# Kernel optimization log

Measured on AMD Instinct MI355X. Metric: run time of the kernel, lower is better.

Reference implementation:

```python
import jax, jax.numpy as jnp
import numpy as np

N, B, LMAX, M, D, KV, H = 12288, 4, 4096, 1024, 256, 512, 8
EPS = 1e-5


def layernorm(x, g, b):
    mu = jnp.mean(x, axis=-1, keepdims=True)
    var = jnp.mean(jnp.square(x - mu), axis=-1, keepdims=True)
    return (x - mu) * jax.lax.rsqrt(var + EPS) * g + b


def setup_inputs() -> dict:
    key = jax.random.key(0)
    ks = jax.random.split(key, 8)
    s = 0.02
    F = jax.random.normal(ks[0], (N, D), jnp.float32)
    batch_idx = jnp.sort(jax.random.randint(ks[1], (N,), 0, B, dtype=jnp.int32))
    y = jax.random.normal(ks[2], (B, M, KV), jnp.float32)
    Wq = jax.random.normal(ks[3], (D, D), jnp.float32) * s
    Wk = jax.random.normal(ks[4], (D, KV), jnp.float32) * s
    Wv = jax.random.normal(ks[5], (D, KV), jnp.float32) * s
    Wo = jax.random.normal(ks[6], (D, D), jnp.float32) * s
    zb = jnp.zeros((D,), jnp.float32)
    return dict(F=F, batch_idx=batch_idx, y=y,
                Wq=Wq, bq=zb, Wk=Wk, bk=zb, Wv=Wv, bv=zb, Wo=Wo, bo=zb,
                ln_g=jnp.ones((D,), jnp.float32), ln_b=zb, Lmax=LMAX)


def reference(F, batch_idx, y, Wq, bq, Wk, bk, Wv, bv, Wo, bo, ln_g, ln_b, Lmax):
    Bn, Mn, _ = y.shape
    n, d = F.shape
    # sparse_to_dense: scatter points into [B, Lmax, D] by (batch, position-in-batch)
    counts = jax.ops.segment_sum(jnp.ones((n,), jnp.int32), batch_idx, num_segments=Bn)
    starts = jnp.cumsum(counts) - counts                      # first row of each batch
    pos = jnp.arange(n, dtype=jnp.int32) - starts[batch_idx]  # intra-batch position
    xd = jnp.zeros((Bn, Lmax, d), F.dtype).at[batch_idx, pos].set(F)
    # pre-norm (shared LayerNorm params, reused again post-residual)
    q_in = layernorm(xd, ln_g, ln_b)
    # multi-head cross-attention (no key padding mask: mask arg is None here)
    dh = d // H
    q = (q_in @ Wq.T + bq).reshape(Bn, Lmax, H, dh)
    k = (y @ Wk.T + bk).reshape(Bn, Mn, H, dh)
    v = (y @ Wv.T + bv).reshape(Bn, Mn, H, dh)
    scores = jnp.einsum('blhd,bmhd->bhlm', q, k) / jnp.sqrt(jnp.float32(dh))
    p = jax.nn.softmax(scores, axis=-1)
    o = jnp.einsum('bhlm,bmhd->blhd', p, v).reshape(Bn, Lmax, d)
    attn = o @ Wo.T + bo
    # residual on the (normed) query, then the SAME LayerNorm again
    res = layernorm(q_in + attn, ln_g, ln_b)
    # dense_to_sparse: gather valid rows back (row-major order == input order)
    return res[batch_idx, pos]
```

## Files before the change

### kernel.cpp

```cpp
#include <hip/hip_runtime.h>

constexpr int NP = 12288;
constexpr int NB = 4;
constexpr int MC = 1024;
constexpr int DM = 256;
constexpr int KVD = 512;
constexpr int NH = 8;
constexpr int DH = 32;

typedef __bf16 bf16x8 __attribute__((ext_vector_type(8)));
typedef __bf16 bf16x4 __attribute__((ext_vector_type(4)));
typedef float f32x4v __attribute__((ext_vector_type(4)));

__device__ inline bf16x8 pack8(float4 a, float4 b) {
    bf16x8 r;
    r[0] = (__bf16)a.x; r[1] = (__bf16)a.y; r[2] = (__bf16)a.z; r[3] = (__bf16)a.w;
    r[4] = (__bf16)b.x; r[5] = (__bf16)b.y; r[6] = (__bf16)b.z; r[7] = (__bf16)b.w;
    return r;
}

__global__ __launch_bounds__(256) void k_prep(const float* __restrict__ F,
        const int* __restrict__ bidx,
        const float* __restrict__ wq, const float* __restrict__ wk,
        const float* __restrict__ wv, const float* __restrict__ wo,
        const float* __restrict__ g, const float* __restrict__ bb,
        int* __restrict__ starts,
        __bf16* wqb, __bf16* wkb, __bf16* wvb, __bf16* wob,
        __bf16* __restrict__ q_in_b) {
    const int bid = blockIdx.x, t = threadIdx.x;
    if (bid == 0) {
        if (t > NB) return;
        int lo = 0, hi = NP;
        while (lo < hi) { int mid = (lo + hi) >> 1; if (bidx[mid] < t) lo = mid + 1; else hi = mid; }
        starts[t] = lo;
        return;
    }
    if (bid <= 384) {
        size_t i = ((size_t)(bid - 1) * 256 + t) * 4;
        const float* s; __bf16* d; size_t off;
        if      (i < 65536)  { s = wq; d = wqb; off = 0; }
        else if (i < 196608) { s = wk; d = wkb; off = 65536; }
        else if (i < 327680) { s = wv; d = wvb; off = 196608; }
        else                 { s = wo; d = wob; off = 327680; }
        size_t j = i - off;
        float4 v = *(const float4*)&s[j];
        bf16x4 o; o[0] = (__bf16)v.x; o[1] = (__bf16)v.y; o[2] = (__bf16)v.z; o[3] = (__bf16)v.w;
        *(bf16x4*)&d[j] = o;
        return;
    }
    const int w = t >> 6, l = t & 63;
    size_t row = (size_t)(bid - 385) * 4 + w;
    float4 v = *(const float4*)&F[row * DM + l * 4];
    float s = v.x + v.y + v.z + v.w;
#pragma unroll
    for (int o2 = 1; o2 < 64; o2 <<= 1) s += __shfl_xor(s, o2);
    float mu = s * (1.f / DM);
    float4 d = {v.x - mu, v.y - mu, v.z - mu, v.w - mu};
    float ss = d.x * d.x + d.y * d.y + d.z * d.z + d.w * d.w;
#pragma unroll
    for (int o2 = 1; o2 < 64; o2 <<= 1) ss += __shfl_xor(ss, o2);
    float rr = rsqrtf(ss * (1.f / DM) + 1e-5f);
    float4 gg = *(const float4*)&g[l * 4];
    float4 bv = *(const float4*)&bb[l * 4];
    bf16x4 ob4;
    ob4[0] = (__bf16)(d.x * rr * gg.x + bv.x);
    ob4[1] = (__bf16)(d.y * rr * gg.y + bv.y);
    ob4[2] = (__bf16)(d.z * rr * gg.z + bv.z);
    ob4[3] = (__bf16)(d.w * rr * gg.w + bv.w);
    *(bf16x4*)&q_in_b[row * DM + l * 4] = ob4;
}

__global__ __launch_bounds__(256) void k_qkv(const __bf16* __restrict__ Aq,
        const __bf16* __restrict__ Wq, const float* __restrict__ bq,
        const float* __restrict__ Yf,
        const __bf16* __restrict__ Wk, const float* __restrict__ bk,
        const __bf16* __restrict__ Wv, const float* __restrict__ bv,
        __bf16* __restrict__ Qo, __bf16* __restrict__ Kf,
        __bf16* __restrict__ Vf, float qscale) {
    __shared__ __bf16 As[128][68];
    __shared__ __bf16 Bs[64][68];
    const int t = threadIdx.x;
    const int w = t >> 6, l = t & 63, lg = l >> 4, ln = l & 15;
    const int wr = w >> 1, wc = w & 1;
    const int ar = t >> 3, ac8 = (t & 7) * 8;
    if ((int)blockIdx.x < 384) {
        f32x4v acc[4][2] = {};
        const int K = DM;
        const int col0 = (blockIdx.x & 3) * 64, row0 = (blockIdx.x >> 2) * 128;
        bf16x8 ra0, ra1, ra2, ra3, rb0, rb1;
#define LOADGQ(K0) \
        ra0 = *(const bf16x8*)&Aq[(size_t)(row0 + ar) * K + (K0) + ac8];        \
        ra1 = *(const bf16x8*)&Aq[(size_t)(row0 + ar + 32) * K + (K0) + ac8];   \
        ra2 = *(const bf16x8*)&Aq[(size_t)(row0 + ar + 64) * K + (K0) + ac8];   \
        ra3 = *(const bf16x8*)&Aq[(size_t)(row0 + ar + 96) * K + (K0) + ac8];   \
        rb0 = *(const bf16x8*)&Wq[(size_t)(col0 + ar) * K + (K0) + ac8];        \
        rb1 = *(const bf16x8*)&Wq[(size_t)(col0 + ar + 32) * K + (K0) + ac8];
        LOADGQ(0)
        for (int k0 = 0; k0 < K; k0 += 64) {
            __syncthreads();
            *(bf16x8*)&As[ar][ac8] = ra0;
            *(bf16x8*)&As[ar + 32][ac8] = ra1;
            *(bf16x8*)&As[ar + 64][ac8] = ra2;
            *(bf16x8*)&As[ar + 96][ac8] = ra3;
            *(bf16x8*)&Bs[ar][ac8] = rb0;
            *(bf16x8*)&Bs[ar + 32][ac8] = rb1;
            __syncthreads();
            if (k0 + 64 < K) { LOADGQ(k0 + 64) }
#pragma unroll
            for (int kk = 0; kk < 2; ++kk) {
                bf16x8 bfr[2];
#pragma unroll
                for (int ni = 0; ni < 2; ++ni) {
                    bf16x4 lo = *(const bf16x4*)&Bs[wc * 32 + ni * 16 + ln][kk * 32 + lg * 4];
                    bf16x4 hi = *(const bf16x4*)&Bs[wc * 32 + ni * 16 + ln][kk * 32 + 16 + lg * 4];
                    bfr[ni] = __builtin_shufflevector(lo, hi, 0, 1, 2, 3, 4, 5, 6, 7);
                }
#pragma unroll
                for (int mi = 0; mi < 4; ++mi) {
                    bf16x4 lo = *(const bf16x4*)&As[wr * 64 + mi * 16 + ln][kk * 32 + lg * 4];
                    bf16x4 hi = *(const bf16x4*)&As[wr * 64 + mi * 16 + ln][kk * 32 + 16 + lg * 4];
                    bf16x8 af = __builtin_shufflevector(lo, hi, 0, 1, 2, 3, 4, 5, 6, 7);
#pragma unroll
                    for (int ni = 0; ni < 2; ++ni)
                        acc[mi][ni] = __builtin_amdgcn_mfma_f32_16x16x32_bf16(bfr[ni], af, acc[mi][ni], 0, 0, 0);
                }
            }
        }
#undef LOADGQ
#pragma unroll
        for (int mi = 0; mi < 4; ++mi)
#pragma unroll
            for (int ni = 0; ni < 2; ++ni) {
                int cb = col0 + wc * 32 + ni * 16 + 4 * lg;
                float4 b4 = *(const float4*)&bq[cb];
                size_t row = row0 + wr * 64 + mi * 16 + ln;
                bf16x4 pk;
                pk[0] = (__bf16)((acc[mi][ni][0] + b4.x) * qscale);
                pk[1] = (__bf16)((acc[mi][ni][1] + b4.y) * qscale);
                pk[2] = (__bf16)((acc[mi][ni][2] + b4.z) * qscale);
                pk[3] = (__bf16)((acc[mi][ni][3] + b4.w) * qscale);
                *(bf16x4*)&Qo[row * DM + cb] = pk;
            }
    } else {
        f32x4v acc[2][2] = {};
        const int K = KVD;
        const int idx = blockIdx.x - 384;
        const int bx = idx & 7, row0 = (idx >> 3) * 64;
        const bool vpath = bx >= 4;
        const int col0 = (bx & 3) * 64;
        const __bf16* Wm = vpath ? Wv : Wk;
        const float* bi = vpath ? bv : bk;
        float4 a0, a1, a2, a3;
        bf16x8 rb0, rb1;
#define LOADGK(K0) \
        a0 = *(const float4*)&Yf[(size_t)(row0 + ar) * K + (K0) + ac8];            \
        a1 = *(const float4*)&Yf[(size_t)(row0 + ar) * K + (K0) + ac8 + 4];        \
        a2 = *(const float4*)&Yf[(size_t)(row0 + ar + 32) * K + (K0) + ac8];       \
        a3 = *(const float4*)&Yf[(size_t)(row0 + ar + 32) * K + (K0) + ac8 + 4];   \
        rb0 = *(const bf16x8*)&Wm[(size_t)(col0 + ar) * K + (K0) + ac8];           \
        rb1 = *(const bf16x8*)&Wm[(size_t)(col0 + ar + 32) * K + (K0) + ac8];
        LOADGK(0)
        for (int k0 = 0; k0 < K; k0 += 64) {
            __syncthreads();
            *(bf16x8*)&As[ar][ac8] = pack8(a0, a1);
            *(bf16x8*)&As[ar + 32][ac8] = pack8(a2, a3);
            *(bf16x8*)&Bs[ar][ac8] = rb0;
            *(bf16x8*)&Bs[ar + 32][ac8] = rb1;
            __syncthreads();
            if (k0 + 64 < K) { LOADGK(k0 + 64) }
#pragma unroll
            for (int kk = 0; kk < 2; ++kk) {
                bf16x8 bfr[2];
#pragma unroll
                for (int ni = 0; ni < 2; ++ni) {
                    bf16x4 lo = *(const bf16x4*)&Bs[wc * 32 + ni * 16 + ln][kk * 32 + lg * 4];
                    bf16x4 hi = *(const bf16x4*)&Bs[wc * 32 + ni * 16 + ln][kk * 32 + 16 + lg * 4];
                    bfr[ni] = __builtin_shufflevector(lo, hi, 0, 1, 2, 3, 4, 5, 6, 7);
                }
#pragma unroll
                for (int mi = 0; mi < 2; ++mi) {
                    bf16x4 lo = *(const bf16x4*)&As[wr * 32 + mi * 16 + ln][kk * 32 + lg * 4];
                    bf16x4 hi = *(const bf16x4*)&As[wr * 32 + mi * 16 + ln][kk * 32 + 16 + lg * 4];
                    bf16x8 af = __builtin_shufflevector(lo, hi, 0, 1, 2, 3, 4, 5, 6, 7);
#pragma unroll
                    for (int ni = 0; ni < 2; ++ni) {
                        if (vpath)
                            acc[mi][ni] = __builtin_amdgcn_mfma_f32_16x16x32_bf16(af, bfr[ni], acc[mi][ni], 0, 0, 0);
                        else
                            acc[mi][ni] = __builtin_amdgcn_mfma_f32_16x16x32_bf16(bfr[ni], af, acc[mi][ni], 0, 0, 0);
                    }
                }
            }
        }
#undef LOADGK
        if (vpath) {
            const int h = (col0 + wc * 32) >> 5;
#pragma unroll
            for (int mi = 0; mi < 2; ++mi)
#pragma unroll
                for (int ni = 0; ni < 2; ++ni) {
                    int C = col0 + wc * 32 + ni * 16 + ln;
                    int nt = (C >> 4) & 1;
                    float bvv = bi[C];
                    int m = row0 + wr * 32 + mi * 16 + 4 * lg;
                    int b = m >> 10, mlocal = m & 1023;
                    int mhg = mlocal >> 5;
                    bf16x4 pk;
#pragma unroll
                    for (int r = 0; r < 4; ++r) pk[r] = (__bf16)(acc[mi][ni][r] + bvv);
                    *(bf16x4*)&Vf[(size_t)(((b * NH + h) * 32 + mhg) * 2 + nt) * 512 + l * 8 + mi * 4] = pk;
                }
        } else {
            const int h = (col0 + wc * 32) >> 5;
#pragma unroll
            for (int mi = 0; mi < 2; ++mi) {
                int m = row0 + wr * 32 + mi * 16 + ln;
                int b = m >> 10, mlocal = m & 1023;
                int msg = mlocal >> 4;
#pragma unroll
                for (int ni = 0; ni < 2; ++ni) {
                    int cb = col0 + wc * 32 + ni * 16 + 4 * lg;
                    float4 b4 = *(const float4*)&bi[cb];
                    bf16x4 pk;
                    pk[0] = (__bf16)(acc[mi][ni][0] + b4.x);
                    pk[1] = (__bf16)(acc[mi][ni][1] + b4.y);
                    pk[2] = (__bf16)(acc[mi][ni][2] + b4.z);
                    pk[3] = (__bf16)(acc[mi][ni][3] + b4.w);
                    *(bf16x4*)&Kf[(size_t)((b * NH + h) * 64 + msg) * 512 + l * 8 + ni * 4] = pk;
                }
            }
        }
    }
}

__global__ __launch_bounds__(256) void k_attn_mfma(const __bf16* __restrict__ q,
        const __bf16* __restrict__ Kf, const __bf16* __restrict__ Vf,
        const int* __restrict__ starts, __bf16* __restrict__ o) {
    const int b = blockIdx.z, h = blockIdx.y;
    const int r0 = starts[b] + blockIdx.x * 128;
    const int rend = starts[b + 1];
    if (r0 >= rend) return;
    const int nr = min(128, rend - r0);

    const int t = threadIdx.x;
    const int w = t >> 6, l = t & 63, lg = l >> 4, ln = l & 15;

    const __bf16* kfb = Kf + (size_t)(b * NH + h) * 32768;
    const __bf16* vfb = Vf + (size_t)(b * NH + h) * 32768;

    const int qr0 = min(r0 + w * 32 + ln, NP - 1);
    const int qr1 = min(r0 + w * 32 + 16 + ln, NP - 1);
    const __bf16* qp0 = q + (size_t)qr0 * DM + h * DH;
    const __bf16* qp1 = q + (size_t)qr1 * DM + h * DH;
    bf16x8 qf0 = __builtin_shufflevector(*(const bf16x4*)(qp0 + lg * 4),
                                         *(const bf16x4*)(qp0 + 16 + lg * 4),
                                         0, 1, 2, 3, 4, 5, 6, 7);
    bf16x8 qf1 = __builtin_shufflevector(*(const bf16x4*)(qp1 + lg * 4),
                                         *(const bf16x4*)(qp1 + 16 + lg * 4),
                                         0, 1, 2, 3, 4, 5, 6, 7);

    f32x4v OaccA[2] = {{0.f, 0.f, 0.f, 0.f}, {0.f, 0.f, 0.f, 0.f}};
    f32x4v OaccB[2] = {{0.f, 0.f, 0.f, 0.f}, {0.f, 0.f, 0.f, 0.f}};
    float lsA4[4] = {0.f, 0.f, 0.f, 0.f};
    float lsB4[4] = {0.f, 0.f, 0.f, 0.f};

    for (int mt = 0; mt < 8; ++mt) {
        bf16x8 kfr[8];
#pragma unroll
        for (int ms = 0; ms < 8; ++ms)
            kfr[ms] = *(const bf16x8*)&kfb[(size_t)((mt * 8 + ms) * 64 + l) * 8];
        f32x4v S0[8], S1[8];
        __builtin_amdgcn_s_setprio(1);
#pragma unroll
        for (int ms = 0; ms < 8; ++ms) {
            S0[ms] = __builtin_amdgcn_mfma_f32_16x16x32_bf16(
                kfr[ms], qf0, (f32x4v){0.f, 0.f, 0.f, 0.f}, 0, 0, 0);
            S1[ms] = __builtin_amdgcn_mfma_f32_16x16x32_bf16(
                kfr[ms], qf1, (f32x4v){0.f, 0.f, 0.f, 0.f}, 0, 0, 0);
        }
        __builtin_amdgcn_s_setprio(0);
        bf16x8 vfr[8];
#pragma unroll
        for (int i = 0; i < 8; ++i)
            vfr[i] = *(const bf16x8*)&vfb[(size_t)((mt * 8 + i) * 64 + l) * 8];
        bf16x8 pa0[4], pa1[4];
#pragma unroll
        for (int ms = 0; ms < 8; ++ms) {
            const int mh = ms >> 1, j0 = (ms & 1) * 4;
#pragma unroll
            for (int r = 0; r < 4; ++r) {
                float e = __builtin_amdgcn_exp2f(S0[ms][r]);
                lsA4[r] += e;
                pa0[mh][j0 + r] = (__bf16)e;
            }
#pragma unroll
            for (int r = 0; r < 4; ++r) {
                float e = __builtin_amdgcn_exp2f(S1[ms][r]);
                lsB4[r] += e;
                pa1[mh][j0 + r] = (__bf16)e;
            }
        }
        __builtin_amdgcn_s_setprio(1);
#pragma unroll
        for (int mh = 0; mh < 4; ++mh)
#pragma unroll
            for (int nt = 0; nt < 2; ++nt) {
                OaccA[nt] = __builtin_amdgcn_mfma_f32_16x16x32_bf16(pa0[mh], vfr[mh * 2 + nt], OaccA[nt], 0, 0, 0);
                OaccB[nt] = __builtin_amdgcn_mfma_f32_16x16x32_bf16(pa1[mh], vfr[mh * 2 + nt], OaccB[nt], 0, 0, 0);
            }
        __builtin_amdgcn_s_setprio(0);
    }
    float lsA = (lsA4[0] + lsA4[1]) + (lsA4[2] + lsA4[3]);
    float lsB = (lsB4[0] + lsB4[1]) + (lsB4[2] + lsB4[3]);
    lsA += __shfl_xor(lsA, 16); lsA += __shfl_xor(lsA, 32);
    lsB += __shfl_xor(lsB, 16); lsB += __shfl_xor(lsB, 32);
    float invA = 1.0f / lsA, invB = 1.0f / lsB;
    float ivA[4], ivB[4];
#pragma unroll
    for (int r = 0; r < 4; ++r) {
        ivA[r] = __shfl(invA, 4 * lg + r);
        ivB[r] = __shfl(invB, 4 * lg + r);
    }
#pragma unroll
    for (int r = 0; r < 4; ++r) {
        int rlocA = w * 32 + 4 * lg + r;
        if (rlocA < nr) {
            size_t base = (size_t)(r0 + rlocA) * DM + h * DH + ln;
            o[base] = (__bf16)(OaccA[0][r] * ivA[r]);
            o[base + 16] = (__bf16)(OaccA[1][r] * ivA[r]);
        }
        int rlocB = w * 32 + 16 + 4 * lg + r;
        if (rlocB < nr) {
            size_t base = (size_t)(r0 + rlocB) * DM + h * DH + ln;
            o[base] = (__bf16)(OaccB[0][r] * ivB[r]);
            o[base + 16] = (__bf16)(OaccB[1][r] * ivB[r]);
        }
    }
}

__global__ __launch_bounds__(256) void k_gemmo_ln(const __bf16* __restrict__ A,
        const __bf16* __restrict__ W, const float* __restrict__ bias,
        const __bf16* __restrict__ resid, const float* __restrict__ g,
        const float* __restrict__ bb, float* __restrict__ out) {
    __shared__ __bf16 As[32][68];
    __shared__ __bf16 Bs[256][68];
    __shared__ float red[32][4][2];
    const int t = threadIdx.x;
    const int w = t >> 6, l = t & 63, lg = l >> 4, ln = l & 15;
    const int row0 = blockIdx.x * 32;
    const int ar = t >> 3, ac8 = (t & 7) * 8;
    f32x4v acc[2][4] = {};
    for (int k0 = 0; k0 < DM; k0 += 64) {
        __syncthreads();
        *(bf16x8*)&As[ar][ac8] = *(const bf16x8*)&A[(size_t)(row0 + ar) * DM + k0 + ac8];
#pragma unroll
        for (int j = 0; j < 8; ++j)
            *(bf16x8*)&Bs[ar + 32 * j][ac8] = *(const bf16x8*)&W[(size_t)(ar + 32 * j) * DM + k0 + ac8];
        __syncthreads();
#pragma unroll
        for (int kk = 0; kk < 2; ++kk) {
            bf16x8 bfr[4];
#pragma unroll
            for (int ni = 0; ni < 4; ++ni) {
                bf16x4 lo = *(const bf16x4*)&Bs[w * 64 + ni * 16 + ln][kk * 32 + lg * 4];
                bf16x4 hi = *(const bf16x4*)&Bs[w * 64 + ni * 16 + ln][kk * 32 + 16 + lg * 4];
                bfr[ni] = __builtin_shufflevector(lo, hi, 0, 1, 2, 3, 4, 5, 6, 7);
            }
#pragma unroll
            for (int mi = 0; mi < 2; ++mi) {
                bf16x4 lo = *(const bf16x4*)&As[mi * 16 + ln][kk * 32 + lg * 4];
                bf16x4 hi = *(const bf16x4*)&As[mi * 16 + ln][kk * 32 + 16 + lg * 4];
                bf16x8 af = __builtin_shufflevector(lo, hi, 0, 1, 2, 3, 4, 5, 6, 7);
#pragma unroll
                for (int ni = 0; ni < 4; ++ni)
                    acc[mi][ni] = __builtin_amdgcn_mfma_f32_16x16x32_bf16(bfr[ni], af, acc[mi][ni], 0, 0, 0);
            }
        }
    }
    float s[2] = {0.f, 0.f}, ss[2] = {0.f, 0.f};
#pragma unroll
    for (int mi = 0; mi < 2; ++mi) {
        int row = row0 + mi * 16 + ln;
#pragma unroll
        for (int ni = 0; ni < 4; ++ni) {
            int cb = w * 64 + ni * 16 + lg * 4;
            float4 b4 = *(const float4*)&bias[cb];
            bf16x4 rv = *(const bf16x4*)&resid[(size_t)row * DM + cb];
            float z0 = acc[mi][ni][0] + b4.x + (float)rv[0];
            float z1 = acc[mi][ni][1] + b4.y + (float)rv[1];
            float z2 = acc[mi][ni][2] + b4.z + (float)rv[2];
            float z3 = acc[mi][ni][3] + b4.w + (float)rv[3];
            acc[mi][ni][0] = z0; acc[mi][ni][1] = z1;
            acc[mi][ni][2] = z2; acc[mi][ni][3] = z3;
            s[mi] += (z0 + z1) + (z2 + z3);
            ss[mi] += (z0 * z0 + z1 * z1) + (z2 * z2 + z3 * z3);
        }
    }
#pragma unroll
    for (int mi = 0; mi < 2; ++mi) {
        s[mi] += __shfl_xor(s[mi], 16);  s[mi] += __shfl_xor(s[mi], 32);
        ss[mi] += __shfl_xor(ss[mi], 16); ss[mi] += __shfl_xor(ss[mi], 32);
    }
    if (l < 16) {
#pragma unroll
        for (int mi = 0; mi < 2; ++mi) {
            red[mi * 16 + ln][w][0] = s[mi];
            red[mi * 16 + ln][w][1] = ss[mi];
        }
    }
    __syncthreads();
#pragma unroll
    for (int mi = 0; mi < 2; ++mi) {
        int rloc = mi * 16 + ln;
        float su = (red[rloc][0][0] + red[rloc][1][0]) + (red[rloc][2][0] + red[rloc][3][0]);
        float sq = (red[rloc][0][1] + red[rloc][1][1]) + (red[rloc][2][1] + red[rloc][3][1]);
        float mu = su * (1.f / DM);
        float var = sq * (1.f / DM) - mu * mu;
        float rs = rsqrtf(var + 1e-5f);
        size_t row = row0 + rloc;
#pragma unroll
        for (int ni = 0; ni < 4; ++ni) {
            int cb = w * 64 + ni * 16 + lg * 4;
            float4 g4 = *(const float4*)&g[cb];
            float4 bb4 = *(const float4*)&bb[cb];
            float4 o4;
            o4.x = (acc[mi][ni][0] - mu) * rs * g4.x + bb4.x;
            o4.y = (acc[mi][ni][1] - mu) * rs * g4.y + bb4.y;
            o4.z = (acc[mi][ni][2] - mu) * rs * g4.z + bb4.z;
            o4.w = (acc[mi][ni][3] - mu) * rs * g4.w + bb4.w;
            *(float4*)&out[row * DM + cb] = o4;
        }
    }
}

extern "C" void kernel_launch(void* const* d_in, const int* in_sizes, int n_in,
                              void* d_out, int out_size, void* d_ws, size_t ws_size,
                              hipStream_t stream) {
    const float* F  = (const float*)d_in[0];
    const int* bidx = (const int*)d_in[1];
    const float* y  = (const float*)d_in[2];
    const float* Wq = (const float*)d_in[3];
    const float* bq = (const float*)d_in[4];
    const float* Wk = (const float*)d_in[5];
    const float* bk = (const float*)d_in[6];
    const float* Wv = (const float*)d_in[7];
    const float* bv = (const float*)d_in[8];
    const float* Wo = (const float*)d_in[9];
    const float* bo = (const float*)d_in[10];
    const float* lg = (const float*)d_in[11];
    const float* lb = (const float*)d_in[12];
    float* out = (float*)d_out;

    char* ws = (char*)d_ws;
    __bf16* q_in_b = (__bf16*)ws;   ws += (size_t)NP * DM * 2;
    __bf16* qb     = (__bf16*)ws;   ws += (size_t)NP * DM * 2;
    __bf16* ob     = (__bf16*)ws;   ws += (size_t)NP * DM * 2;
    __bf16* Kf     = (__bf16*)ws;   ws += (size_t)NB * MC * DM * 2;
    __bf16* Vf     = (__bf16*)ws;   ws += (size_t)NB * DM * MC * 2;
    __bf16* Wq_b   = (__bf16*)ws;   ws += (size_t)DM * DM * 2;
    __bf16* Wk_b   = (__bf16*)ws;   ws += (size_t)DM * KVD * 2;
    __bf16* Wv_b   = (__bf16*)ws;   ws += (size_t)DM * KVD * 2;
    __bf16* Wo_b   = (__bf16*)ws;   ws += (size_t)DM * DM * 2;
    int* starts    = (int*)ws;

    const float qscale = 0.17677669529663687f * 1.4426950408889634f;

    k_prep<<<1 + 384 + NP / 4, 256, 0, stream>>>(F, bidx, Wq, Wk, Wv, Wo, lg, lb,
            starts, Wq_b, Wk_b, Wv_b, Wo_b, q_in_b);
    k_qkv<<<384 + 512, 256, 0, stream>>>(q_in_b, Wq_b, bq, y, Wk_b, bk, Wv_b, bv,
            qb, Kf, Vf, qscale);
    k_attn_mfma<<<dim3(NP / 128, NH, NB), 256, 0, stream>>>(qb, Kf, Vf, starts, ob);
    k_gemmo_ln<<<NP / 32, 256, 0, stream>>>(ob, Wo_b, bo, q_in_b, lg, lb, out);
}
```

Baseline: 70.70 us.

## Split attention over two key halves and merge partials in output GEMM

The attention grid gains a factor-two split along the key dimension. Each block processes half of the 1024 keys and writes an unnormalised partial output and its per-row exp-sum. The output-projection GEMM loads both partials, adds them, divides by the summed normaliser and then runs its MFMA. This doubles the number of active attention blocks and halves each block's serial loop, at the cost of writing and reading an extra partial output buffer and keeping unnormalised values in bf16.

```diff
diff --git a/kernel.cpp b/kernel.cpp
--- a/kernel.cpp
+++ b/kernel.cpp
@@ -235,8 +235,9 @@
 
 __global__ __launch_bounds__(256) void k_attn_mfma(const __bf16* __restrict__ q,
         const __bf16* __restrict__ Kf, const __bf16* __restrict__ Vf,
-        const int* __restrict__ starts, __bf16* __restrict__ o) {
-    const int b = blockIdx.z, h = blockIdx.y;
+        const int* __restrict__ starts, __bf16* __restrict__ op,
+        float* __restrict__ lsums) {
+    const int z = blockIdx.z, b = z >> 1, half = z & 1, h = blockIdx.y;
     const int r0 = starts[b] + blockIdx.x * 128;
     const int rend = starts[b + 1];
     if (r0 >= rend) return;
@@ -245,8 +246,8 @@
     const int t = threadIdx.x;
     const int w = t >> 6, l = t & 63, lg = l >> 4, ln = l & 15;
 
-    const __bf16* kfb = Kf + (size_t)(b * NH + h) * 32768;
-    const __bf16* vfb = Vf + (size_t)(b * NH + h) * 32768;
+    const __bf16* kfb = Kf + (size_t)(b * NH + h) * 32768 + half * 16384;
+    const __bf16* vfb = Vf + (size_t)(b * NH + h) * 32768 + half * 16384;
 
     const int qr0 = min(r0 + w * 32 + ln, NP - 1);
     const int qr1 = min(r0 + w * 32 + 16 + ln, NP - 1);
@@ -264,7 +265,7 @@
     float lsA4[4] = {0.f, 0.f, 0.f, 0.f};
     float lsB4[4] = {0.f, 0.f, 0.f, 0.f};
 
-    for (int mt = 0; mt < 8; ++mt) {
+    for (int mt = 0; mt < 4; ++mt) {
         bf16x8 kfr[8];
 #pragma unroll
         for (int ms = 0; ms < 8; ++ms)
@@ -314,31 +315,31 @@
     float lsB = (lsB4[0] + lsB4[1]) + (lsB4[2] + lsB4[3]);
     lsA += __shfl_xor(lsA, 16); lsA += __shfl_xor(lsA, 32);
     lsB += __shfl_xor(lsB, 16); lsB += __shfl_xor(lsB, 32);
-    float invA = 1.0f / lsA, invB = 1.0f / lsB;
-    float ivA[4], ivB[4];
-#pragma unroll
-    for (int r = 0; r < 4; ++r) {
-        ivA[r] = __shfl(invA, 4 * lg + r);
-        ivB[r] = __shfl(invB, 4 * lg + r);
+    __bf16* oh = op + (size_t)half * NP * DM;
+    if (l < 16) {
+        int rA = w * 32 + ln, rB = rA + 16;
+        if (rA < nr) lsums[((size_t)half * NP + r0 + rA) * NH + h] = lsA;
+        if (rB < nr) lsums[((size_t)half * NP + r0 + rB) * NH + h] = lsB;
     }
 #pragma unroll
     for (int r = 0; r < 4; ++r) {
         int rlocA = w * 32 + 4 * lg + r;
         if (rlocA < nr) {
             size_t base = (size_t)(r0 + rlocA) * DM + h * DH + ln;
-            o[base] = (__bf16)(OaccA[0][r] * ivA[r]);
-            o[base + 16] = (__bf16)(OaccA[1][r] * ivA[r]);
+            oh[base] = (__bf16)OaccA[0][r];
+            oh[base + 16] = (__bf16)OaccA[1][r];
         }
         int rlocB = w * 32 + 16 + 4 * lg + r;
         if (rlocB < nr) {
             size_t base = (size_t)(r0 + rlocB) * DM + h * DH + ln;
-            o[base] = (__bf16)(OaccB[0][r] * ivB[r]);
-            o[base + 16] = (__bf16)(OaccB[1][r] * ivB[r]);
-        }
-    }
-}
-
-__global__ __launch_bounds__(256) void k_gemmo_ln(const __bf16* __restrict__ A,
+            oh[base] = (__bf16)OaccB[0][r];
+            oh[base + 16] = (__bf16)OaccB[1][r];
+        }
+    }
+}
+
+__global__ __launch_bounds__(256) void k_gemmo_ln(const __bf16* __restrict__ O1,
+        const __bf16* __restrict__ O2, const float* __restrict__ L,
         const __bf16* __restrict__ W, const float* __restrict__ bias,
         const __bf16* __restrict__ resid, const float* __restrict__ g,
         const float* __restrict__ bb, float* __restrict__ out) {
@@ -352,7 +353,18 @@
     f32x4v acc[2][4] = {};
     for (int k0 = 0; k0 < DM; k0 += 64) {
         __syncthreads();
-        *(bf16x8*)&As[ar][ac8] = *(const bf16x8*)&A[(size_t)(row0 + ar) * DM + k0 + ac8];
+        {
+            int row = row0 + ar;
+            int hh = (k0 + ac8) >> 5;
+            float inv = 1.0f / (L[(size_t)row * NH + hh] + L[(size_t)(NP + row) * NH + hh]);
+            bf16x8 o1 = *(const bf16x8*)&O1[(size_t)row * DM + k0 + ac8];
+            bf16x8 o2 = *(const bf16x8*)&O2[(size_t)row * DM + k0 + ac8];
+            bf16x8 s8;
+#pragma unroll
+            for (int j = 0; j < 8; ++j)
+                s8[j] = (__bf16)(((float)o1[j] + (float)o2[j]) * inv);
+            *(bf16x8*)&As[ar][ac8] = s8;
+        }
 #pragma unroll
         for (int j = 0; j < 8; ++j)
             *(bf16x8*)&Bs[ar + 32 * j][ac8] = *(const bf16x8*)&W[(size_t)(ar + 32 * j) * DM + k0 + ac8];
@@ -454,13 +466,14 @@
     char* ws = (char*)d_ws;
     __bf16* q_in_b = (__bf16*)ws;   ws += (size_t)NP * DM * 2;
     __bf16* qb     = (__bf16*)ws;   ws += (size_t)NP * DM * 2;
-    __bf16* ob     = (__bf16*)ws;   ws += (size_t)NP * DM * 2;
+    __bf16* obp    = (__bf16*)ws;   ws += (size_t)2 * NP * DM * 2;
     __bf16* Kf     = (__bf16*)ws;   ws += (size_t)NB * MC * DM * 2;
     __bf16* Vf     = (__bf16*)ws;   ws += (size_t)NB * DM * MC * 2;
     __bf16* Wq_b   = (__bf16*)ws;   ws += (size_t)DM * DM * 2;
     __bf16* Wk_b   = (__bf16*)ws;   ws += (size_t)DM * KVD * 2;
     __bf16* Wv_b   = (__bf16*)ws;   ws += (size_t)DM * KVD * 2;
     __bf16* Wo_b   = (__bf16*)ws;   ws += (size_t)DM * DM * 2;
+    float* lsums   = (float*)ws;    ws += (size_t)2 * NP * NH * 4;
     int* starts    = (int*)ws;
 
     const float qscale = 0.17677669529663687f * 1.4426950408889634f;
@@ -469,6 +482,8 @@
             starts, Wq_b, Wk_b, Wv_b, Wo_b, q_in_b);
     k_qkv<<<384 + 512, 256, 0, stream>>>(q_in_b, Wq_b, bq, y, Wk_b, bk, Wv_b, bv,
             qb, Kf, Vf, qscale);
-    k_attn_mfma<<<dim3(NP / 128, NH, NB), 256, 0, stream>>>(qb, Kf, Vf, starts, ob);
-    k_gemmo_ln<<<NP / 32, 256, 0, stream>>>(ob, Wo_b, bo, q_in_b, lg, lb, out);
-}
+    k_attn_mfma<<<dim3(NP / 128, NH, NB * 2), 256, 0, stream>>>(qb, Kf, Vf, starts,
+            obp, lsums);
+    k_gemmo_ln<<<NP / 32, 256, 0, stream>>>(obp, obp + (size_t)NP * DM, lsums,
+            Wo_b, bo, q_in_b, lg, lb, out);
+}
```

Result: slower. 75.61 us (+7.0%).

## Fuse LayerNorm and weight casting into the QKV projection kernel

Applied to the files above, without the earlier changes.

The separate prep kernel is removed. The Q-projection blocks now compute per-row LayerNorm statistics themselves and normalise F on the fly while staging tiles into LDS. Only the col0==0 blocks write q_in_b for the later residual. The K/V paths read fp32 weights and convert them in registers, while Wo conversion and the batch-start search run in extra blocks of the same launch. This saves one launch and a round trip of q_in_b and bf16 weights through memory, but the Q path loses its register prefetch and each of the four column blocks re-reads F. Variance is now computed with the single-pass E[x²]-mu² formula.

```diff
diff --git a/kernel.cpp b/kernel.cpp
--- a/kernel.cpp
+++ b/kernel.cpp
@@ -19,93 +19,86 @@
     return r;
 }
 
-__global__ __launch_bounds__(256) void k_prep(const float* __restrict__ F,
+__global__ __launch_bounds__(256) void k_qkv(const float* __restrict__ F,
+        const float* __restrict__ Wqf, const float* __restrict__ bq,
+        const float* __restrict__ Yf,
+        const float* __restrict__ Wkf, const float* __restrict__ bk,
+        const float* __restrict__ Wvf, const float* __restrict__ bv,
+        const float* __restrict__ Wof,
+        const float* __restrict__ lng, const float* __restrict__ lnb,
         const int* __restrict__ bidx,
-        const float* __restrict__ wq, const float* __restrict__ wk,
-        const float* __restrict__ wv, const float* __restrict__ wo,
-        const float* __restrict__ g, const float* __restrict__ bb,
-        int* __restrict__ starts,
-        __bf16* wqb, __bf16* wkb, __bf16* wvb, __bf16* wob,
-        __bf16* __restrict__ q_in_b) {
-    const int bid = blockIdx.x, t = threadIdx.x;
-    if (bid == 0) {
-        if (t > NB) return;
-        int lo = 0, hi = NP;
-        while (lo < hi) { int mid = (lo + hi) >> 1; if (bidx[mid] < t) lo = mid + 1; else hi = mid; }
-        starts[t] = lo;
-        return;
-    }
-    if (bid <= 384) {
-        size_t i = ((size_t)(bid - 1) * 256 + t) * 4;
-        const float* s; __bf16* d; size_t off;
-        if      (i < 65536)  { s = wq; d = wqb; off = 0; }
-        else if (i < 196608) { s = wk; d = wkb; off = 65536; }
-        else if (i < 327680) { s = wv; d = wvb; off = 196608; }
-        else                 { s = wo; d = wob; off = 327680; }
-        size_t j = i - off;
-        float4 v = *(const float4*)&s[j];
-        bf16x4 o; o[0] = (__bf16)v.x; o[1] = (__bf16)v.y; o[2] = (__bf16)v.z; o[3] = (__bf16)v.w;
-        *(bf16x4*)&d[j] = o;
-        return;
-    }
-    const int w = t >> 6, l = t & 63;
-    size_t row = (size_t)(bid - 385) * 4 + w;
-    float4 v = *(const float4*)&F[row * DM + l * 4];
-    float s = v.x + v.y + v.z + v.w;
-#pragma unroll
-    for (int o2 = 1; o2 < 64; o2 <<= 1) s += __shfl_xor(s, o2);
-    float mu = s * (1.f / DM);
-    float4 d = {v.x - mu, v.y - mu, v.z - mu, v.w - mu};
-    float ss = d.x * d.x + d.y * d.y + d.z * d.z + d.w * d.w;
-#pragma unroll
-    for (int o2 = 1; o2 < 64; o2 <<= 1) ss += __shfl_xor(ss, o2);
-    float rr = rsqrtf(ss * (1.f / DM) + 1e-5f);
-    float4 gg = *(const float4*)&g[l * 4];
-    float4 bv = *(const float4*)&bb[l * 4];
-    bf16x4 ob4;
-    ob4[0] = (__bf16)(d.x * rr * gg.x + bv.x);
-    ob4[1] = (__bf16)(d.y * rr * gg.y + bv.y);
-    ob4[2] = (__bf16)(d.z * rr * gg.z + bv.z);
-    ob4[3] = (__bf16)(d.w * rr * gg.w + bv.w);
-    *(bf16x4*)&q_in_b[row * DM + l * 4] = ob4;
-}
-
-__global__ __launch_bounds__(256) void k_qkv(const __bf16* __restrict__ Aq,
-        const __bf16* __restrict__ Wq, const float* __restrict__ bq,
-        const float* __restrict__ Yf,
-        const __bf16* __restrict__ Wk, const float* __restrict__ bk,
-        const __bf16* __restrict__ Wv, const float* __restrict__ bv,
-        __bf16* __restrict__ Qo, __bf16* __restrict__ Kf,
-        __bf16* __restrict__ Vf, float qscale) {
+        __bf16* __restrict__ q_in_b, __bf16* __restrict__ Qo,
+        __bf16* __restrict__ Kf, __bf16* __restrict__ Vf,
+        __bf16* __restrict__ Wo_b, int* __restrict__ starts, float qscale) {
     __shared__ __bf16 As[128][68];
     __shared__ __bf16 Bs[64][68];
+    __shared__ float mu_s[128], rr_s[128];
     const int t = threadIdx.x;
     const int w = t >> 6, l = t & 63, lg = l >> 4, ln = l & 15;
     const int wr = w >> 1, wc = w & 1;
     const int ar = t >> 3, ac8 = (t & 7) * 8;
-    if ((int)blockIdx.x < 384) {
+    const int bid = blockIdx.x;
+    if (bid < 384) {
+        const int row0 = (bid >> 2) * 128, col0 = (bid & 3) * 64;
+        {
+            const int c0 = (t & 7) * 32;
+            for (int rg = 0; rg < 4; ++rg) {
+                int row = row0 + ar + rg * 32;
+                float s = 0.f, ss = 0.f;
+#pragma unroll
+                for (int j = 0; j < 8; ++j) {
+                    float4 v = *(const float4*)&F[(size_t)row * DM + c0 + 4 * j];
+                    s += (v.x + v.y) + (v.z + v.w);
+                    ss += (v.x * v.x + v.y * v.y) + (v.z * v.z + v.w * v.w);
+                }
+                s += __shfl_xor(s, 1); ss += __shfl_xor(ss, 1);
+                s += __shfl_xor(s, 2); ss += __shfl_xor(ss, 2);
+                s += __shfl_xor(s, 4); ss += __shfl_xor(ss, 4);
+                if ((t & 7) == 0) {
+                    float mu = s * (1.f / DM);
+                    float var = ss * (1.f / DM) - mu * mu;
+                    mu_s[ar + rg * 32] = mu;
+                    rr_s[ar + rg * 32] = rsqrtf(var + 1e-5f);
+                }
+            }
+        }
         f32x4v acc[4][2] = {};
-        const int K = DM;
-        const int col0 = (blockIdx.x & 3) * 64, row0 = (blockIdx.x >> 2) * 128;
-        bf16x8 ra0, ra1, ra2, ra3, rb0, rb1;
-#define LOADGQ(K0) \
-        ra0 = *(const bf16x8*)&Aq[(size_t)(row0 + ar) * K + (K0) + ac8];        \
-        ra1 = *(const bf16x8*)&Aq[(size_t)(row0 + ar + 32) * K + (K0) + ac8];   \
-        ra2 = *(const bf16x8*)&Aq[(size_t)(row0 + ar + 64) * K + (K0) + ac8];   \
-        ra3 = *(const bf16x8*)&Aq[(size_t)(row0 + ar + 96) * K + (K0) + ac8];   \
-        rb0 = *(const bf16x8*)&Wq[(size_t)(col0 + ar) * K + (K0) + ac8];        \
-        rb1 = *(const bf16x8*)&Wq[(size_t)(col0 + ar + 32) * K + (K0) + ac8];
-        LOADGQ(0)
-        for (int k0 = 0; k0 < K; k0 += 64) {
+        for (int k0 = 0; k0 < DM; k0 += 64) {
             __syncthreads();
-            *(bf16x8*)&As[ar][ac8] = ra0;
-            *(bf16x8*)&As[ar + 32][ac8] = ra1;
-            *(bf16x8*)&As[ar + 64][ac8] = ra2;
-            *(bf16x8*)&As[ar + 96][ac8] = ra3;
-            *(bf16x8*)&Bs[ar][ac8] = rb0;
-            *(bf16x8*)&Bs[ar + 32][ac8] = rb1;
+            float4 g0 = *(const float4*)&lng[k0 + ac8];
+            float4 g1 = *(const float4*)&lng[k0 + ac8 + 4];
+            float4 e0 = *(const float4*)&lnb[k0 + ac8];
+            float4 e1 = *(const float4*)&lnb[k0 + ac8 + 4];
+#pragma unroll
+            for (int rg = 0; rg < 4; ++rg) {
+                int rl = ar + rg * 32;
+                float mu = mu_s[rl], rr = rr_s[rl];
+                size_t base = (size_t)(row0 + rl) * DM + k0 + ac8;
+                float4 v0 = *(const float4*)&F[base];
+                float4 v1 = *(const float4*)&F[base + 4];
+                bf16x8 o;
+                o[0] = (__bf16)((v0.x - mu) * rr * g0.x + e0.x);
+                o[1] = (__bf16)((v0.y - mu) * rr * g0.y + e0.y);
+                o[2] = (__bf16)((v0.z - mu) * rr * g0.z + e0.z);
+                o[3] = (__bf16)((v0.w - mu) * rr * g0.w + e0.w);
+                o[4] = (__bf16)((v1.x - mu) * rr * g1.x + e1.x);
+                o[5] = (__bf16)((v1.y - mu) * rr * g1.y + e1.y);
+                o[6] = (__bf16)((v1.z - mu) * rr * g1.z + e1.z);
+                o[7] = (__bf16)((v1.w - mu) * rr * g1.w + e1.w);
+                *(bf16x8*)&As[rl][ac8] = o;
+                if (col0 == 0) *(bf16x8*)&q_in_b[base] = o;
+            }
+            {
+                size_t wb = (size_t)(col0 + ar) * DM + k0 + ac8;
+                float4 w0 = *(const float4*)&Wqf[wb];
+                float4 w1 = *(const float4*)&Wqf[wb + 4];
+                *(bf16x8*)&Bs[ar][ac8] = pack8(w0, w1);
+                wb = (size_t)(col0 + ar + 32) * DM + k0 + ac8;
+                w0 = *(const float4*)&Wqf[wb];
+                w1 = *(const float4*)&Wqf[wb + 4];
+                *(bf16x8*)&Bs[ar + 32][ac8] = pack8(w0, w1);
+            }
             __syncthreads();
-            if (k0 + 64 < K) { LOADGQ(k0 + 64) }
 #pragma unroll
             for (int kk = 0; kk < 2; ++kk) {
                 bf16x8 bfr[2];
@@ -126,7 +119,6 @@
                 }
             }
         }
-#undef LOADGQ
 #pragma unroll
         for (int mi = 0; mi < 4; ++mi)
 #pragma unroll
@@ -141,31 +133,32 @@
                 pk[3] = (__bf16)((acc[mi][ni][3] + b4.w) * qscale);
                 *(bf16x4*)&Qo[row * DM + cb] = pk;
             }
-    } else {
+    } else if (bid < 896) {
         f32x4v acc[2][2] = {};
         const int K = KVD;
-        const int idx = blockIdx.x - 384;
+        const int idx = bid - 384;
         const int bx = idx & 7, row0 = (idx >> 3) * 64;
         const bool vpath = bx >= 4;
         const int col0 = (bx & 3) * 64;
-        const __bf16* Wm = vpath ? Wv : Wk;
+        const float* Wmf = vpath ? Wvf : Wkf;
         const float* bi = vpath ? bv : bk;
-        float4 a0, a1, a2, a3;
-        bf16x8 rb0, rb1;
+        float4 a0, a1, a2, a3, w0, w1, w2, w3;
 #define LOADGK(K0) \
         a0 = *(const float4*)&Yf[(size_t)(row0 + ar) * K + (K0) + ac8];            \
         a1 = *(const float4*)&Yf[(size_t)(row0 + ar) * K + (K0) + ac8 + 4];        \
         a2 = *(const float4*)&Yf[(size_t)(row0 + ar + 32) * K + (K0) + ac8];       \
         a3 = *(const float4*)&Yf[(size_t)(row0 + ar + 32) * K + (K0) + ac8 + 4];   \
-        rb0 = *(const bf16x8*)&Wm[(size_t)(col0 + ar) * K + (K0) + ac8];           \
-        rb1 = *(const bf16x8*)&Wm[(size_t)(col0 + ar + 32) * K + (K0) + ac8];
+        w0 = *(const float4*)&Wmf[(size_t)(col0 + ar) * K + (K0) + ac8];           \
+        w1 = *(const float4*)&Wmf[(size_t)(col0 + ar) * K + (K0) + ac8 + 4];       \
+        w2 = *(const float4*)&Wmf[(size_t)(col0 + ar + 32) * K + (K0) + ac8];      \
+        w3 = *(const float4*)&Wmf[(size_t)(col0 + ar + 32) * K + (K0) + ac8 + 4];
         LOADGK(0)
         for (int k0 = 0; k0 < K; k0 += 64) {
             __syncthreads();
             *(bf16x8*)&As[ar][ac8] = pack8(a0, a1);
             *(bf16x8*)&As[ar + 32][ac8] = pack8(a2, a3);
-            *(bf16x8*)&Bs[ar][ac8] = rb0;
-            *(bf16x8*)&Bs[ar + 32][ac8] = rb1;
+            *(bf16x8*)&Bs[ar][ac8] = pack8(w0, w1);
+            *(bf16x8*)&Bs[ar + 32][ac8] = pack8(w2, w3);
             __syncthreads();
             if (k0 + 64 < K) { LOADGK(k0 + 64) }
 #pragma unroll
@@ -229,6 +222,17 @@
                     *(bf16x4*)&Kf[(size_t)((b * NH + h) * 64 + msg) * 512 + l * 8 + ni * 4] = pk;
                 }
             }
+        }
+    } else if (bid < 928) {
+        size_t i = ((size_t)(bid - 896) * 256 + t) * 8;
+        float4 v0 = *(const float4*)&Wof[i];
+        float4 v1 = *(const float4*)&Wof[i + 4];
+        *(bf16x8*)&Wo_b[i] = pack8(v0, v1);
+    } else {
+        if (t <= NB) {
+            int lo = 0, hi = NP;
+            while (lo < hi) { int mid = (lo + hi) >> 1; if (bidx[mid] < t) lo = mid + 1; else hi = mid; }
+            starts[t] = lo;
         }
     }
 }
@@ -457,18 +461,13 @@
     __bf16* ob     = (__bf16*)ws;   ws += (size_t)NP * DM * 2;
     __bf16* Kf     = (__bf16*)ws;   ws += (size_t)NB * MC * DM * 2;
     __bf16* Vf     = (__bf16*)ws;   ws += (size_t)NB * DM * MC * 2;
-    __bf16* Wq_b   = (__bf16*)ws;   ws += (size_t)DM * DM * 2;
-    __bf16* Wk_b   = (__bf16*)ws;   ws += (size_t)DM * KVD * 2;
-    __bf16* Wv_b   = (__bf16*)ws;   ws += (size_t)DM * KVD * 2;
     __bf16* Wo_b   = (__bf16*)ws;   ws += (size_t)DM * DM * 2;
     int* starts    = (int*)ws;
 
     const float qscale = 0.17677669529663687f * 1.4426950408889634f;
 
-    k_prep<<<1 + 384 + NP / 4, 256, 0, stream>>>(F, bidx, Wq, Wk, Wv, Wo, lg, lb,
-            starts, Wq_b, Wk_b, Wv_b, Wo_b, q_in_b);
-    k_qkv<<<384 + 512, 256, 0, stream>>>(q_in_b, Wq_b, bq, y, Wk_b, bk, Wv_b, bv,
-            qb, Kf, Vf, qscale);
+    k_qkv<<<929, 256, 0, stream>>>(F, Wq, bq, y, Wk, bk, Wv, bv, Wo, lg, lb, bidx,
+            q_in_b, qb, Kf, Vf, Wo_b, starts, qscale);
     k_attn_mfma<<<dim3(NP / 128, NH, NB), 256, 0, stream>>>(qb, Kf, Vf, starts, ob);
     k_gemmo_ln<<<NP / 32, 256, 0, stream>>>(ob, Wo_b, bo, q_in_b, lg, lb, out);
 }
```

After: 75.79 us. +7.2%, slower.
